# Performance work log

Measured on AMD Instinct MI355X. Metric: run time of the kernel, lower is better.

## Reference

```python
import jax, jax.numpy as jnp
import numpy as np

ALPHA = 0.2  # LeakyReLU negative slope
EDGE_NUM = 3


def _gat(q_nodes, v, adj, a_q, a_v):
    # q_nodes: (b,n,d_hidden), v: (b,n,d_model), adj: (b,n,n)
    # e_ij = LeakyReLU(a_q . h_i + a_v . v_j)  (decomposition of a^T[h_i;v_j])
    s_q = jnp.einsum('bnd,d->bn', q_nodes, a_q)
    s_v = jnp.einsum('bne,e->bn', v, a_v)
    e = jax.nn.leaky_relu(s_q[:, :, None] + s_v[:, None, :], negative_slope=ALPHA)
    e = jnp.where(adj > 0, e, -1e9)
    attn = jax.nn.softmax(e, axis=-1)           # (b,n,n)
    return jnp.einsum('bij,bje->bie', attn, v)  # (b,n,d_model)


def setup_inputs() -> dict:
    key = jax.random.key(0)
    ks = jax.random.split(key, 16)
    b, n, dh, dm = 8, 1024, 512, 512
    s = 0.02
    inp = {
        'nodes': jax.random.normal(ks[0], (b, n, dh), dtype=jnp.float32),
        'mask': jax.random.randint(ks[1], (2, b, n, n), 0, 2, dtype=jnp.int32),
        'node_type': jax.random.randint(ks[2], (b, n), 0, 5, dtype=jnp.int64),
        # edge-typed linears (bias=False), stacked over 3 edge types
        'W_in': jax.random.normal(ks[3], (EDGE_NUM, dh, dm), dtype=jnp.float32) * s,
        'W_out': jax.random.normal(ks[4], (EDGE_NUM, dh, dm), dtype=jnp.float32) * s,
        # GAT attention vectors, split into query / value halves
        'a_in_q': jax.random.normal(ks[5], (dh,), dtype=jnp.float32) * s,
        'a_in_v': jax.random.normal(ks[6], (dm,), dtype=jnp.float32) * s,
        'a_out_q': jax.random.normal(ks[7], (dh,), dtype=jnp.float32) * s,
        'a_out_v': jax.random.normal(ks[8], (dm,), dtype=jnp.float32) * s,
        # GGNN propagator (reset / update / transform)
        'W_r': jax.random.normal(ks[9], (3 * dm, dm), dtype=jnp.float32) * s,
        'b_r': jnp.zeros((dm,), dtype=jnp.float32),
        'W_z': jax.random.normal(ks[10], (3 * dm, dm), dtype=jnp.float32) * s,
        'b_z': jnp.zeros((dm,), dtype=jnp.float32),
        'W_t': jax.random.normal(ks[11], (3 * dm, dm), dtype=jnp.float32) * s,
        'b_t': jnp.zeros((dm,), dtype=jnp.float32),
    }
    return inp


def reference(nodes, mask, node_type, W_in, W_out, a_in_q, a_in_v, a_out_q, a_out_v,
              W_r, b_r, W_z, b_z, W_t, b_t):
    # type masks for tags 2,3,4 -> (3,b,n)
    tags = jnp.arange(2, 2 + EDGE_NUM, dtype=node_type.dtype)
    tmask = (node_type[None, :, :] == tags[:, None, None]).astype(nodes.dtype)
    # edge-typed linear + masked sum over edge types
    node_in = jnp.sum(jnp.einsum('bnd,tde->tbne', nodes, W_in) * tmask[..., None], axis=0)
    node_out = jnp.sum(jnp.einsum('bnd,tde->tbne', nodes, W_out) * tmask[..., None], axis=0)
    # GAT-style masked attention (in / out edges); dropout = identity (eval)
    h_in = _gat(nodes, node_in, mask[0], a_in_q, a_in_v)
    h_out = _gat(nodes, node_out, mask[1], a_out_q, a_out_v)
    # GGNN gated propagator
    a = jnp.concatenate([h_in, h_out, nodes], axis=-1)
    r = jax.nn.sigmoid(a @ W_r + b_r)
    z = jax.nn.sigmoid(a @ W_z + b_z)
    joint = jnp.concatenate([h_in, h_out, r * nodes], axis=-1)
    h_hat = jnp.tanh(joint @ W_t + b_t)
    return (1.0 - z) * nodes + z * h_hat
```

## Files before the change

### kernel.cpp

```cpp
#include <hip/hip_runtime.h>
#include <hip/hip_bf16.h>
#include <stdint.h>

typedef unsigned short u16;
typedef __attribute__((ext_vector_type(8))) short bf16x8;
typedef __attribute__((ext_vector_type(4))) float floatx4;

__device__ __forceinline__ float bf2f(u16 v){ return __uint_as_float(((unsigned)v)<<16); }
__device__ __forceinline__ u16 f2bf(float f){
  unsigned u = __float_as_uint(f);
  unsigned r = 0x7fffu + ((u>>16)&1u);
  return (u16)((u+r)>>16);
}
__device__ __forceinline__ float lrelu(float x){ return x > 0.f ? x : 0.2f*x; }
__device__ __forceinline__ float sigm(float t){
  t = fminf(fmaxf(t, -30.f), 30.f);
  return 1.f/(1.f + expf(-t));
}

#define GLOAD16(ldsdst, gsrc) \
  __builtin_amdgcn_global_load_lds((const __attribute__((address_space(1))) void*)(gsrc), \
      (__attribute__((address_space(3))) void*)(ldsdst), 16, 0, 0)

__global__ void k_detect(const u16* __restrict__ nodes_raw,
                         const int* __restrict__ ntype_raw, int* flags)
{
  __shared__ int s_wild, s_nz;
  if (threadIdx.x == 0){ s_wild = 0; s_nz = 0; }
  __syncthreads();
  int wild = 0;
#pragma unroll
  for (int i = 0; i < 16; i++){
    u16 w = nodes_raw[threadIdx.x*16 + i];
    int e = (w >> 7) & 0xFF;
    if (e != 0 && (e < 102 || e > 152)) wild++;
  }
  int nz = 0;
  if (threadIdx.x < 255 && ntype_raw[2*threadIdx.x + 1] != 0) nz = 1;
  atomicAdd(&s_wild, wild);
  atomicAdd(&s_nz, nz);
  __syncthreads();
  if (threadIdx.x == 0){
    flags[0] = (s_wild > 1024) ? 1 : 0;
    flags[1] = (s_nz == 0) ? 1 : 0;
  }
}

struct CanonDesc {
  const void* src[13];
  u16*        dst[13];
  int startBlk[13];
  int n4[13];
};
__global__ __launch_bounds__(256)
void k_canon_all(CanonDesc d, const int* __restrict__ flags)
{
  int blk = blockIdx.x;
  int seg = 0;
#pragma unroll
  for (int s = 1; s < 13; s++) if (blk >= d.startBlk[s]) seg = s;
  int i = (blk - d.startBlk[seg])*256 + threadIdx.x;
  if (i >= d.n4[seg]) return;
  if (flags[0]) {
    float4 v = ((const float4*)d.src[seg])[i];
    ushort4 o2;
    o2.x = f2bf(v.x); o2.y = f2bf(v.y); o2.z = f2bf(v.z); o2.w = f2bf(v.w);
    ((ushort4*)d.dst[seg])[i] = o2;
  } else {
    ((uint2*)d.dst[seg])[i] = ((const uint2*)d.src[seg])[i];
  }
}

__global__ void k_build_idx(const int* __restrict__ ntype, const int* __restrict__ flags,
                            int* __restrict__ idx, int* __restrict__ cnt)
{
  __shared__ int c[3];
  if (threadIdx.x < 3) c[threadIdx.x] = 0;
  __syncthreads();
  const int i64 = flags[1];
  for (int i = threadIdx.x; i < 8192; i += 256){
    int t = i64 ? ntype[2*i] : ntype[i];
    if (t >= 2 && t <= 4){
      int p = atomicAdd(&c[t-2], 1);
      idx[(t-2)*8192 + p] = i;
    }
  }
  __syncthreads();
  if (threadIdx.x < 3) cnt[threadIdx.x] = c[threadIdx.x];
}

template<class Epi>
__global__ __launch_bounds__(256)
void gemm_bt(const u16* __restrict__ A, int ldA, long sAz,
             const u16* __restrict__ B, int ldB, long sBz,
             int K, Epi epi)
{
  __shared__ __align__(16) u16 As[128][32];
  __shared__ __align__(16) u16 Bs[128][32];
  const int bn = blockIdx.x, bm = blockIdx.y, bz = blockIdx.z;
  const int tid  = threadIdx.x;
  const int lane = tid & 63;
  const int wave = tid >> 6;
  const int wm = (wave & 1) << 6;
  const int wn = (wave >> 1) << 6;
  const int mrow = lane & 15;
  const int quad = lane >> 4;

  const u16* Ab = A + (long)bz*sAz + (long)bm*128*ldA;
  const u16* Bb = B + (long)bz*sBz + (long)bn*128*ldB;
  const int srow = tid >> 2;
  const int scol = (tid & 3) << 3;
  const u16* gA0 = Ab + (long)srow*ldA + scol;
  const u16* gA1 = Ab + (long)(srow+64)*ldA + scol;
  const u16* gB0 = Bb + (long)srow*ldB + scol;
  const u16* gB1 = Bb + (long)(srow+64)*ldB + scol;
  u16* lA0 = &As[srow][scol];
  u16* lA1 = &As[srow+64][scol];
  u16* lB0 = &Bs[srow][scol];
  u16* lB1 = &Bs[srow+64][scol];

  floatx4 acc[4][4];
#pragma unroll
  for (int i=0;i<4;i++)
#pragma unroll
    for (int j=0;j<4;j++) acc[i][j] = 0.f;

  for (int k0 = 0; k0 < K; k0 += 32) {
    GLOAD16(lA0, gA0); GLOAD16(lA1, gA1);
    GLOAD16(lB0, gB0); GLOAD16(lB1, gB1);
    gA0 += 32; gA1 += 32; gB0 += 32; gB1 += 32;
    asm volatile("s_waitcnt vmcnt(0)" ::: "memory");
    __syncthreads();
    bf16x8 af[4], bfr[4];
#pragma unroll
    for (int i=0;i<4;i++) af[i]  = *(const bf16x8*)&As[wm + i*16 + mrow][quad*8];
#pragma unroll
    for (int i=0;i<4;i++) bfr[i] = *(const bf16x8*)&Bs[wn + i*16 + mrow][quad*8];
#pragma unroll
    for (int mi=0;mi<4;mi++)
#pragma unroll
      for (int ni=0;ni<4;ni++)
        acc[mi][ni] = __builtin_amdgcn_mfma_f32_16x16x32_bf16(af[mi], bfr[ni], acc[mi][ni], 0,0,0);
    __syncthreads();
  }

#pragma unroll
  for (int mi=0;mi<4;mi++)
#pragma unroll
    for (int ni=0;ni<4;ni++) {
      const int col  = (bn<<7) + wn + ni*16 + mrow;
      const int row0 = (bm<<7) + wm + mi*16 + quad*4;
#pragma unroll
      for (int r=0;r<4;r++)
        epi(row0 + r, col, bz, acc[mi][ni][r]);
    }
}

__global__ __launch_bounds__(256)
void gemm_typed(const u16* __restrict__ A, const u16* __restrict__ B,
                const int* __restrict__ idx, const int* __restrict__ cnt,
                u16* __restrict__ node_in, u16* __restrict__ node_out)
{
  const int bz = blockIdx.z;
  const int count = cnt[bz];
  const int m0 = blockIdx.y << 7;
  if (m0 >= count) return;
  __shared__ __align__(16) u16 As[128][32];
  __shared__ __align__(16) u16 Bs[128][32];
  const int bn = blockIdx.x;
  const int tid  = threadIdx.x;
  const int lane = tid & 63;
  const int wave = tid >> 6;
  const int wm = (wave & 1) << 6;
  const int wn = (wave >> 1) << 6;
  const int mrow = lane & 15;
  const int quad = lane >> 4;
  const int* myidx = idx + bz*8192;

  const int srow = tid >> 2;
  const int scol = (tid & 3) << 3;
  int r0i = m0 + srow;      if (r0i >= count) r0i = m0;
  int r1i = m0 + srow + 64; if (r1i >= count) r1i = m0;
  const u16* gA0 = A + (long)myidx[r0i]*512 + scol;
  const u16* gA1 = A + (long)myidx[r1i]*512 + scol;
  const u16* Bb = B + (long)bz*1024*512 + (long)bn*128*512;
  const u16* gB0 = Bb + (long)srow*512 + scol;
  const u16* gB1 = Bb + (long)(srow+64)*512 + scol;
  u16* lA0 = &As[srow][scol];
  u16* lA1 = &As[srow+64][scol];
  u16* lB0 = &Bs[srow][scol];
  u16* lB1 = &Bs[srow+64][scol];

  floatx4 acc[4][4];
#pragma unroll
  for (int i=0;i<4;i++)
#pragma unroll
    for (int j=0;j<4;j++) acc[i][j] = 0.f;

  for (int k0 = 0; k0 < 512; k0 += 32) {
    GLOAD16(lA0, gA0); GLOAD16(lA1, gA1);
    GLOAD16(lB0, gB0); GLOAD16(lB1, gB1);
    gA0 += 32; gA1 += 32; gB0 += 32; gB1 += 32;
    asm volatile("s_waitcnt vmcnt(0)" ::: "memory");
    __syncthreads();
    bf16x8 af[4], bfr[4];
#pragma unroll
    for (int i=0;i<4;i++) af[i]  = *(const bf16x8*)&As[wm + i*16 + mrow][quad*8];
#pragma unroll
    for (int i=0;i<4;i++) bfr[i] = *(const bf16x8*)&Bs[wn + i*16 + mrow][quad*8];
#pragma unroll
    for (int mi=0;mi<4;mi++)
#pragma unroll
      for (int ni=0;ni<4;ni++)
        acc[mi][ni] = __builtin_amdgcn_mfma_f32_16x16x32_bf16(af[mi], bfr[ni], acc[mi][ni], 0,0,0);
    __syncthreads();
  }

#pragma unroll
  for (int mi=0;mi<4;mi++) {
    const int lr0 = wm + mi*16 + quad*4;
#pragma unroll
    for (int r=0;r<4;r++) {
      const int lr = lr0 + r;
      if (m0 + lr >= count) continue;
      const long orig = myidx[m0 + lr];
#pragma unroll
      for (int ni=0;ni<4;ni++) {
        const int col = (bn<<7) + wn + ni*16 + mrow;
        u16 h = f2bf(acc[mi][ni][r]);
        if (col < 512) node_in [orig*512 + col]       = h;
        else           node_out[orig*512 + (col-512)] = h;
      }
    }
  }
}

struct EpiPV {
  const float* inv_l; u16* X; int colOff;
  __device__ void operator()(int row, int col, int bz, float v) const {
    long gr = (long)bz*1024 + row;
    X[gr*2048 + colOff + col] = f2bf(v * inv_l[gr]);
  }
};
struct EpiG1 {
  const u16* nodes; const u16* b_r; const u16* b_z; u16* X; u16* zbuf;
  __device__ void operator()(int row, int col, int bz, float v) const {
    if (col < 512) {
      float r = sigm(v + bf2f(b_r[col]));
      X[(long)row*2048 + 1536 + col] = f2bf(r * bf2f(nodes[(long)row*512 + col]));
    } else {
      int c = col - 512;
      zbuf[(long)row*512 + c] = f2bf(sigm(v + bf2f(b_z[c])));
    }
  }
};
struct EpiG2 {
  const u16* zbuf; const u16* nodes; const u16* b_t; const int* flags; void* out;
  __device__ void operator()(int row, int col, int bz, float v) const {
    long idx = (long)row*512 + col;
    float t = fminf(fmaxf(v + bf2f(b_t[col]), -15.f), 15.f);
    float h = tanhf(t);
    float z = bf2f(zbuf[idx]);
    float nv = bf2f(nodes[idx]);
    float o2 = (1.f - z)*nv + z*h;
    if (flags[0]) ((float*)out)[idx] = o2;
    else          ((u16*)out)[idx]   = f2bf(o2);
  }
};

__global__ __launch_bounds__(256)
void k_transpose(u16* __restrict__ dst, int ldD, long dzs,
                 const u16* __restrict__ src, int ldS, long szs)
{
  __shared__ u16 tile[32][33];
  src += (long)blockIdx.z * szs;
  dst += (long)blockIdx.z * dzs;
  const int c0 = blockIdx.x*32, r0 = blockIdx.y*32;
  const int tx = threadIdx.x, ty = threadIdx.y;
#pragma unroll
  for (int i=0;i<32;i+=8)
    tile[ty+i][tx] = src[(long)(r0+ty+i)*ldS + c0 + tx];
  __syncthreads();
#pragma unroll
  for (int i=0;i<32;i+=8)
    dst[(long)(c0+ty+i)*ldD + r0 + tx] = tile[tx][ty+i];
}

struct TrDesc { const u16* src[3]; u16* dst[3]; int rot[3]; };
__global__ __launch_bounds__(256)
void k_wtrans(TrDesc d)
{
  __shared__ u16 tile[32][33];
  const int z = blockIdx.z;
  const u16* src = d.src[z];
  u16* dst = d.dst[z];
  const int c0 = blockIdx.x*32, r0 = blockIdx.y*32;
  const int tx = threadIdx.x, ty = threadIdx.y;
#pragma unroll
  for (int i=0;i<32;i+=8)
    tile[ty+i][tx] = src[(long)(r0+ty+i)*512 + c0 + tx];
  __syncthreads();
  const int k0 = (r0 + d.rot[z]) % 1536;
#pragma unroll
  for (int i=0;i<32;i+=8)
    dst[(long)(c0+ty+i)*1536 + k0 + tx] = tile[tx][ty+i];
}

__global__ __launch_bounds__(256)
void k_vtrans(const u16* __restrict__ nin, const u16* __restrict__ nout,
              u16* __restrict__ vin, u16* __restrict__ vout)
{
  __shared__ u16 tile[32][33];
  const int z = blockIdx.z;
  const int b = z & 7;
  const u16* src = (z < 8 ? nin : nout) + (long)b*1024*512;
  u16* dst = (z < 8 ? vin : vout) + (long)b*512*1024;
  const int c0 = blockIdx.x*32, r0 = blockIdx.y*32;
  const int tx = threadIdx.x, ty = threadIdx.y;
#pragma unroll
  for (int i=0;i<32;i+=8)
    tile[ty+i][tx] = src[(long)(r0+ty+i)*512 + c0 + tx];
  __syncthreads();
#pragma unroll
  for (int i=0;i<32;i+=8)
    dst[(long)(c0+ty+i)*1024 + r0 + tx] = tile[tx][ty+i];
}

__global__ __launch_bounds__(256)
void k_copyX(const u16* __restrict__ nodes, u16* __restrict__ X)
{
  long idx = (long)blockIdx.x*256 + threadIdx.x;
  long r = idx >> 6;
  int  c = (int)(idx & 63) << 3;
  *(uint4*)&X[r*2048 + c] = *(const uint4*)&nodes[r*512 + c];
}

__device__ __forceinline__ void load8f(float* f, const u16* p){
  uint4 q = *(const uint4*)p;
  unsigned w[4] = {q.x, q.y, q.z, q.w};
#pragma unroll
  for (int i=0;i<4;i++){ f[2*i] = bf2f((u16)(w[i]&0xffffu)); f[2*i+1] = bf2f((u16)(w[i]>>16)); }
}

__global__ __launch_bounds__(256)
void k_svec(const u16* __restrict__ nodes, const u16* __restrict__ nin, const u16* __restrict__ nout,
            const u16* __restrict__ aiq, const u16* __restrict__ aiv,
            const u16* __restrict__ aoq, const u16* __restrict__ aov,
            float* sq_in, float* sq_out, float* sv_in, float* sv_out)
{
  const int lane = threadIdx.x & 63, wave = threadIdx.x >> 6;
  const long row = (long)blockIdx.x*4 + wave;
  const int c = lane << 3;
  float xn[8], xi[8], xo[8], q1[8], v1[8], q2[8], v2[8];
  load8f(xn, nodes + row*512 + c);
  load8f(xi, nin   + row*512 + c);
  load8f(xo, nout  + row*512 + c);
  load8f(q1, aiq + c); load8f(v1, aiv + c);
  load8f(q2, aoq + c); load8f(v2, aov + c);
  float s0=0,s1=0,s2=0,s3=0;
#pragma unroll
  for (int j=0;j<8;j++){ s0 += xn[j]*q1[j]; s1 += xn[j]*q2[j]; s2 += xi[j]*v1[j]; s3 += xo[j]*v2[j]; }
#pragma unroll
  for (int off=32; off; off>>=1){
    s0 += __shfl_xor(s0, off);
    s1 += __shfl_xor(s1, off);
    s2 += __shfl_xor(s2, off);
    s3 += __shfl_xor(s3, off);
  }
  if (lane==0){ sq_in[row]=s0; sq_out[row]=s1; sv_in[row]=s2; sv_out[row]=s3; }
}

__global__ __launch_bounds__(256)
void k_stats(const int* __restrict__ mask, const float* __restrict__ sq,
             const float* __restrict__ sv, u16* __restrict__ P, float* __restrict__ inv_l)
{
  const int lane = threadIdx.x & 63, wave = threadIdx.x >> 6;
  const long row = (long)blockIdx.x*4 + wave;
  const long b = row >> 10;
  const int* mrow = mask + row*1024;
  const float* svb = sv + b*1024;
  const float qs = sq[row];
  float m = -3.0e38f;
#pragma unroll
  for (int it=0; it<8; ++it) {
    int j = it*128 + lane*2;
    int2 mk = *(const int2*)&mrow[j];
    float2 s = *(const float2*)&svb[j];
    float e0 = mk.x > 0 ? lrelu(qs + s.x) : -1e9f;
    float e1 = mk.y > 0 ? lrelu(qs + s.y) : -1e9f;
    m = fmaxf(m, fmaxf(e0, e1));
  }
#pragma unroll
  for (int off=32; off; off>>=1) m = fmaxf(m, __shfl_xor(m, off));
  float l = 0.f;
#pragma unroll
  for (int it=0; it<8; ++it) {
    int j = it*128 + lane*2;
    int2 mk = *(const int2*)&mrow[j];
    float2 s = *(const float2*)&svb[j];
    float e0 = mk.x > 0 ? lrelu(qs + s.x) : -1e9f;
    float e1 = mk.y > 0 ? lrelu(qs + s.y) : -1e9f;
    float p0 = expf(e0 - m), p1 = expf(e1 - m);
    *(unsigned*)&P[row*1024 + j] = (unsigned)f2bf(p0) | ((unsigned)f2bf(p1) << 16);
    l += p0 + p1;
  }
#pragma unroll
  for (int off=32; off; off>>=1) l += __shfl_xor(l, off);
  if (lane==0) inv_l[row] = 1.f / l;
}

extern "C" void kernel_launch(void* const* d_in, const int* in_sizes, int n_in,
                              void* d_out, int out_size, void* d_ws, size_t ws_size,
                              hipStream_t stream)
{
  const void* nodes_r   = d_in[0];
  const int*  mask      = (const int*)d_in[1];
  const int*  ntype     = (const int*)d_in[2];

  char* base = (char*)d_ws;
  size_t o = 0;
  auto alloc = [&](size_t bytes){ void* p = base + o; o += (bytes + 255) & ~size_t(255); return p; };
  int*  flags   = (int*)alloc(256);
  int*  cnt     = (int*)alloc(256);
  int*  idx     = (int*)alloc(3ll*8192*4);
  u16* cn_nodes = (u16*)alloc(8192ll*512*2);
  u16* cn_Win   = (u16*)alloc(3ll*512*512*2);
  u16* cn_Wout  = (u16*)alloc(3ll*512*512*2);
  u16* cn_Wr    = (u16*)alloc(1536ll*512*2);
  u16* cn_Wz    = (u16*)alloc(1536ll*512*2);
  u16* cn_Wt    = (u16*)alloc(1536ll*512*2);
  u16* cn_aiq   = (u16*)alloc(512*2);
  u16* cn_aiv   = (u16*)alloc(512*2);
  u16* cn_aoq   = (u16*)alloc(512*2);
  u16* cn_aov   = (u16*)alloc(512*2);
  u16* cn_br    = (u16*)alloc(512*2);
  u16* cn_bz    = (u16*)alloc(512*2);
  u16* cn_bt    = (u16*)alloc(512*2);
  u16* node_in  = (u16*)alloc(8192ll*512*2);
  u16* node_out = (u16*)alloc(8192ll*512*2);
  u16* VtIn     = (u16*)alloc(8ll*512*1024*2);
  u16* VtOut    = (u16*)alloc(8ll*512*1024*2);
  u16* X        = (u16*)alloc(8192ll*2048*2);
  u16* P        = (u16*)alloc(8ll*1024*1024*2);
  u16* Wio_t    = (u16*)alloc(3ll*1024*512*2);
  u16* Wrz_t    = (u16*)alloc(1024ll*1536*2);
  u16* Wt_t     = (u16*)alloc(512ll*1536*2);
  float* sq_in  = (float*)alloc(8192*4);
  float* sq_out = (float*)alloc(8192*4);
  float* sv_in  = (float*)alloc(8192*4);
  float* sv_out = (float*)alloc(8192*4);
  float* il_in  = (float*)alloc(8192*4);
  float* il_out = (float*)alloc(8192*4);
  u16* zbuf = node_in;

  hipMemsetAsync(node_in, 0, 2ll*8192*512*2, stream);

  k_detect<<<1, 256, 0, stream>>>((const u16*)nodes_r, ntype, flags);

  CanonDesc cd;
  const int canonN[13] = {8192*512, 3*512*512, 3*512*512, 1536*512, 1536*512, 1536*512,
                          512,512,512,512,512,512,512};
  u16* canonDst[13] = {cn_nodes, cn_Win, cn_Wout, cn_Wr, cn_Wz, cn_Wt,
                       cn_aiq, cn_aiv, cn_aoq, cn_aov, cn_br, cn_bz, cn_bt};
  const int canonSrcIdx[13] = {0,3,4,9,11,13,5,6,7,8,10,12,14};
  int blk = 0;
  for (int s=0;s<13;s++){
    cd.src[s] = d_in[canonSrcIdx[s]];
    cd.dst[s] = canonDst[s];
    cd.n4[s]  = canonN[s]/4;
    cd.startBlk[s] = blk;
    blk += (cd.n4[s] + 255)/256;
  }
  k_canon_all<<<blk, 256, 0, stream>>>(cd, flags);

  k_build_idx<<<1, 256, 0, stream>>>(ntype, flags, idx, cnt);

  TrDesc td;
  td.src[0]=cn_Wr; td.src[1]=cn_Wz; td.src[2]=cn_Wt;
  td.dst[0]=Wrz_t; td.dst[1]=Wrz_t + 512ll*1536; td.dst[2]=Wt_t;
  td.rot[0]=512; td.rot[1]=512; td.rot[2]=0;
  k_wtrans<<<dim3(16,48,3), dim3(32,8), 0, stream>>>(td);
  dim3 tb(32,8);
  k_transpose<<<dim3(16,16,3), tb, 0, stream>>>(Wio_t,             512, 1024ll*512, cn_Win,  512, 512ll*512);
  k_transpose<<<dim3(16,16,3), tb, 0, stream>>>(Wio_t + 512ll*512, 512, 1024ll*512, cn_Wout, 512, 512ll*512);

  gemm_typed<<<dim3(8,64,3), 256, 0, stream>>>(cn_nodes, Wio_t, idx, cnt, node_in, node_out);

  k_vtrans<<<dim3(16,32,16), tb, 0, stream>>>(node_in, node_out, VtIn, VtOut);

  k_svec<<<2048, 256, 0, stream>>>(cn_nodes, node_in, node_out, cn_aiq, cn_aiv, cn_aoq, cn_aov,
                                   sq_in, sq_out, sv_in, sv_out);
  k_copyX<<<2048, 256, 0, stream>>>(cn_nodes, X);

  k_stats<<<2048, 256, 0, stream>>>(mask, sq_in, sv_in, P, il_in);
  gemm_bt<<<dim3(4,8,8), 256, 0, stream>>>(P, 1024, 1024ll*1024, VtIn, 1024, 512ll*1024, 1024,
                                           EpiPV{il_in, X, 512});
  k_stats<<<2048, 256, 0, stream>>>(mask + 8ll*1024*1024, sq_out, sv_out, P, il_out);
  gemm_bt<<<dim3(4,8,8), 256, 0, stream>>>(P, 1024, 1024ll*1024, VtOut, 1024, 512ll*1024, 1024,
                                           EpiPV{il_out, X, 1024});

  gemm_bt<<<dim3(8,64,1), 256, 0, stream>>>(X, 2048, 0ll, Wrz_t, 1536, 0ll, 1536,
                                            EpiG1{cn_nodes, cn_br, cn_bz, X, zbuf});
  gemm_bt<<<dim3(4,64,1), 256, 0, stream>>>(X + 512, 2048, 0ll, Wt_t, 1536, 0ll, 1536,
                                            EpiG2{zbuf, cn_nodes, cn_bt, flags, (void*)d_out});
}
```

Before: 435.4 us.

## Double-buffer GEMM LDS tiles, fuse copies and transposes, reorder block grids

The GEMM kernels now use two LDS buffers, so the next K-slice load is issued before the current slice's MFMAs and the trailing barrier per iteration is dropped. The X copy is folded into the canonicalization kernel, and the Win/Wout transposes are merged into one batched k_wtrans launch, removing several launches. Grid dimensions are reordered so adjacent blocks walk M first, or the batch first for the PV GEMMs, to change L2 reuse. k_stats now caches the logits in registers instead of recomputing them, and reads the mask with wider vector loads.

```diff
diff --git a/kernel.cpp b/kernel.cpp
--- a/kernel.cpp
+++ b/kernel.cpp
@@ -53,7 +53,7 @@
   int n4[13];
 };
 __global__ __launch_bounds__(256)
-void k_canon_all(CanonDesc d, const int* __restrict__ flags)
+void k_canon_all(CanonDesc d, u16* __restrict__ X, const int* __restrict__ flags)
 {
   int blk = blockIdx.x;
   int seg = 0;
@@ -61,13 +61,21 @@
   for (int s = 1; s < 13; s++) if (blk >= d.startBlk[s]) seg = s;
   int i = (blk - d.startBlk[seg])*256 + threadIdx.x;
   if (i >= d.n4[seg]) return;
+  uint2 bits;
   if (flags[0]) {
     float4 v = ((const float4*)d.src[seg])[i];
     ushort4 o2;
     o2.x = f2bf(v.x); o2.y = f2bf(v.y); o2.z = f2bf(v.z); o2.w = f2bf(v.w);
-    ((ushort4*)d.dst[seg])[i] = o2;
+    bits = *(uint2*)&o2;
   } else {
-    ((uint2*)d.dst[seg])[i] = ((const uint2*)d.src[seg])[i];
+    bits = ((const uint2*)d.src[seg])[i];
+  }
+  ((uint2*)d.dst[seg])[i] = bits;
+  if (seg == 0) {
+    int e0 = i*4;
+    long r = e0 >> 9;
+    int  c = e0 & 511;
+    *(uint2*)&X[r*2048 + c] = bits;
   }
 }
 
@@ -89,15 +97,17 @@
   if (threadIdx.x < 3) cnt[threadIdx.x] = c[threadIdx.x];
 }
 
-template<class Epi>
+template<int MODE, class Epi>
 __global__ __launch_bounds__(256)
 void gemm_bt(const u16* __restrict__ A, int ldA, long sAz,
              const u16* __restrict__ B, int ldB, long sBz,
              int K, Epi epi)
 {
-  __shared__ __align__(16) u16 As[128][32];
-  __shared__ __align__(16) u16 Bs[128][32];
-  const int bn = blockIdx.x, bm = blockIdx.y, bz = blockIdx.z;
+  __shared__ __align__(16) u16 As[2][128][32];
+  __shared__ __align__(16) u16 Bs[2][128][32];
+  int bm, bn, bz;
+  if (MODE == 0){ bm = blockIdx.x; bn = blockIdx.y; bz = blockIdx.z; }
+  else          { bz = blockIdx.x; bn = blockIdx.y; bm = blockIdx.z; }
   const int tid  = threadIdx.x;
   const int lane = tid & 63;
   const int wave = tid >> 6;
@@ -114,10 +124,6 @@
   const u16* gA1 = Ab + (long)(srow+64)*ldA + scol;
   const u16* gB0 = Bb + (long)srow*ldB + scol;
   const u16* gB1 = Bb + (long)(srow+64)*ldB + scol;
-  u16* lA0 = &As[srow][scol];
-  u16* lA1 = &As[srow+64][scol];
-  u16* lB0 = &Bs[srow][scol];
-  u16* lB1 = &Bs[srow+64][scol];
 
   floatx4 acc[4][4];
 #pragma unroll
@@ -125,23 +131,31 @@
 #pragma unroll
     for (int j=0;j<4;j++) acc[i][j] = 0.f;
 
-  for (int k0 = 0; k0 < K; k0 += 32) {
-    GLOAD16(lA0, gA0); GLOAD16(lA1, gA1);
-    GLOAD16(lB0, gB0); GLOAD16(lB1, gB1);
+  auto issue = [&](int buf){
+    GLOAD16(&As[buf][srow][scol],    gA0);
+    GLOAD16(&As[buf][srow+64][scol], gA1);
+    GLOAD16(&Bs[buf][srow][scol],    gB0);
+    GLOAD16(&Bs[buf][srow+64][scol], gB1);
     gA0 += 32; gA1 += 32; gB0 += 32; gB1 += 32;
+  };
+
+  issue(0);
+  const int nIter = K >> 5;
+  for (int it = 0; it < nIter; ++it) {
+    const int cur = it & 1;
     asm volatile("s_waitcnt vmcnt(0)" ::: "memory");
     __syncthreads();
+    if (it + 1 < nIter) issue(cur ^ 1);
     bf16x8 af[4], bfr[4];
 #pragma unroll
-    for (int i=0;i<4;i++) af[i]  = *(const bf16x8*)&As[wm + i*16 + mrow][quad*8];
-#pragma unroll
-    for (int i=0;i<4;i++) bfr[i] = *(const bf16x8*)&Bs[wn + i*16 + mrow][quad*8];
+    for (int i=0;i<4;i++) af[i]  = *(const bf16x8*)&As[cur][wm + i*16 + mrow][quad*8];
+#pragma unroll
+    for (int i=0;i<4;i++) bfr[i] = *(const bf16x8*)&Bs[cur][wn + i*16 + mrow][quad*8];
 #pragma unroll
     for (int mi=0;mi<4;mi++)
 #pragma unroll
       for (int ni=0;ni<4;ni++)
         acc[mi][ni] = __builtin_amdgcn_mfma_f32_16x16x32_bf16(af[mi], bfr[ni], acc[mi][ni], 0,0,0);
-    __syncthreads();
   }
 
 #pragma unroll
@@ -163,11 +177,11 @@
 {
   const int bz = blockIdx.z;
   const int count = cnt[bz];
-  const int m0 = blockIdx.y << 7;
+  const int m0 = blockIdx.x << 7;
   if (m0 >= count) return;
-  __shared__ __align__(16) u16 As[128][32];
-  __shared__ __align__(16) u16 Bs[128][32];
-  const int bn = blockIdx.x;
+  __shared__ __align__(16) u16 As[2][128][32];
+  __shared__ __align__(16) u16 Bs[2][128][32];
+  const int bn = blockIdx.y;
   const int tid  = threadIdx.x;
   const int lane = tid & 63;
   const int wave = tid >> 6;
@@ -186,10 +200,6 @@
   const u16* Bb = B + (long)bz*1024*512 + (long)bn*128*512;
   const u16* gB0 = Bb + (long)srow*512 + scol;
   const u16* gB1 = Bb + (long)(srow+64)*512 + scol;
-  u16* lA0 = &As[srow][scol];
-  u16* lA1 = &As[srow+64][scol];
-  u16* lB0 = &Bs[srow][scol];
-  u16* lB1 = &Bs[srow+64][scol];
 
   floatx4 acc[4][4];
 #pragma unroll
@@ -197,23 +207,30 @@
 #pragma unroll
     for (int j=0;j<4;j++) acc[i][j] = 0.f;
 
-  for (int k0 = 0; k0 < 512; k0 += 32) {
-    GLOAD16(lA0, gA0); GLOAD16(lA1, gA1);
-    GLOAD16(lB0, gB0); GLOAD16(lB1, gB1);
+  auto issue = [&](int buf){
+    GLOAD16(&As[buf][srow][scol],    gA0);
+    GLOAD16(&As[buf][srow+64][scol], gA1);
+    GLOAD16(&Bs[buf][srow][scol],    gB0);
+    GLOAD16(&Bs[buf][srow+64][scol], gB1);
     gA0 += 32; gA1 += 32; gB0 += 32; gB1 += 32;
+  };
+
+  issue(0);
+  for (int it = 0; it < 16; ++it) {
+    const int cur = it & 1;
     asm volatile("s_waitcnt vmcnt(0)" ::: "memory");
     __syncthreads();
+    if (it + 1 < 16) issue(cur ^ 1);
     bf16x8 af[4], bfr[4];
 #pragma unroll
-    for (int i=0;i<4;i++) af[i]  = *(const bf16x8*)&As[wm + i*16 + mrow][quad*8];
-#pragma unroll
-    for (int i=0;i<4;i++) bfr[i] = *(const bf16x8*)&Bs[wn + i*16 + mrow][quad*8];
+    for (int i=0;i<4;i++) af[i]  = *(const bf16x8*)&As[cur][wm + i*16 + mrow][quad*8];
+#pragma unroll
+    for (int i=0;i<4;i++) bfr[i] = *(const bf16x8*)&Bs[cur][wn + i*16 + mrow][quad*8];
 #pragma unroll
     for (int mi=0;mi<4;mi++)
 #pragma unroll
       for (int ni=0;ni<4;ni++)
         acc[mi][ni] = __builtin_amdgcn_mfma_f32_16x16x32_bf16(af[mi], bfr[ni], acc[mi][ni], 0,0,0);
-    __syncthreads();
   }
 
 #pragma unroll
@@ -268,42 +285,28 @@
   }
 };
 
-__global__ __launch_bounds__(256)
-void k_transpose(u16* __restrict__ dst, int ldD, long dzs,
-                 const u16* __restrict__ src, int ldS, long szs)
-{
-  __shared__ u16 tile[32][33];
-  src += (long)blockIdx.z * szs;
-  dst += (long)blockIdx.z * dzs;
-  const int c0 = blockIdx.x*32, r0 = blockIdx.y*32;
-  const int tx = threadIdx.x, ty = threadIdx.y;
-#pragma unroll
-  for (int i=0;i<32;i+=8)
-    tile[ty+i][tx] = src[(long)(r0+ty+i)*ldS + c0 + tx];
-  __syncthreads();
-#pragma unroll
-  for (int i=0;i<32;i+=8)
-    dst[(long)(c0+ty+i)*ldD + r0 + tx] = tile[tx][ty+i];
-}
-
-struct TrDesc { const u16* src[3]; u16* dst[3]; int rot[3]; };
+struct TrDesc {
+  const u16* src[9]; u16* dst[9]; int rot[9]; int ldD[9]; int rows[9]; int modK[9];
+};
 __global__ __launch_bounds__(256)
 void k_wtrans(TrDesc d)
 {
   __shared__ u16 tile[32][33];
   const int z = blockIdx.z;
+  const int r0 = blockIdx.y*32;
+  if (r0 >= d.rows[z]) return;
   const u16* src = d.src[z];
   u16* dst = d.dst[z];
-  const int c0 = blockIdx.x*32, r0 = blockIdx.y*32;
+  const int c0 = blockIdx.x*32;
   const int tx = threadIdx.x, ty = threadIdx.y;
 #pragma unroll
   for (int i=0;i<32;i+=8)
     tile[ty+i][tx] = src[(long)(r0+ty+i)*512 + c0 + tx];
   __syncthreads();
-  const int k0 = (r0 + d.rot[z]) % 1536;
+  const int k0 = (r0 + d.rot[z]) % d.modK[z];
 #pragma unroll
   for (int i=0;i<32;i+=8)
-    dst[(long)(c0+ty+i)*1536 + k0 + tx] = tile[tx][ty+i];
+    dst[(long)(c0+ty+i)*d.ldD[z] + k0 + tx] = tile[tx][ty+i];
 }
 
 __global__ __launch_bounds__(256)
@@ -324,15 +327,6 @@
 #pragma unroll
   for (int i=0;i<32;i+=8)
     dst[(long)(c0+ty+i)*1024 + r0 + tx] = tile[tx][ty+i];
-}
-
-__global__ __launch_bounds__(256)
-void k_copyX(const u16* __restrict__ nodes, u16* __restrict__ X)
-{
-  long idx = (long)blockIdx.x*256 + threadIdx.x;
-  long r = idx >> 6;
-  int  c = (int)(idx & 63) << 3;
-  *(uint4*)&X[r*2048 + c] = *(const uint4*)&nodes[r*512 + c];
 }
 
 __device__ __forceinline__ void load8f(float* f, const u16* p){
@@ -381,28 +375,30 @@
   const float* svb = sv + b*1024;
   const float qs = sq[row];
   float m = -3.0e38f;
-#pragma unroll
-  for (int it=0; it<8; ++it) {
-    int j = it*128 + lane*2;
-    int2 mk = *(const int2*)&mrow[j];
-    float2 s = *(const float2*)&svb[j];
-    float e0 = mk.x > 0 ? lrelu(qs + s.x) : -1e9f;
-    float e1 = mk.y > 0 ? lrelu(qs + s.y) : -1e9f;
-    m = fmaxf(m, fmaxf(e0, e1));
+  float e[4][4];
+#pragma unroll
+  for (int it=0; it<4; ++it) {
+    int j = it*256 + lane*4;
+    int4 mk = *(const int4*)&mrow[j];
+    float4 s = *(const float4*)&svb[j];
+    e[it][0] = mk.x > 0 ? lrelu(qs + s.x) : -1e9f;
+    e[it][1] = mk.y > 0 ? lrelu(qs + s.y) : -1e9f;
+    e[it][2] = mk.z > 0 ? lrelu(qs + s.z) : -1e9f;
+    e[it][3] = mk.w > 0 ? lrelu(qs + s.w) : -1e9f;
+    m = fmaxf(m, fmaxf(fmaxf(e[it][0], e[it][1]), fmaxf(e[it][2], e[it][3])));
   }
 #pragma unroll
   for (int off=32; off; off>>=1) m = fmaxf(m, __shfl_xor(m, off));
   float l = 0.f;
 #pragma unroll
-  for (int it=0; it<8; ++it) {
-    int j = it*128 + lane*2;
-    int2 mk = *(const int2*)&mrow[j];
-    float2 s = *(const float2*)&svb[j];
-    float e0 = mk.x > 0 ? lrelu(qs + s.x) : -1e9f;
-    float e1 = mk.y > 0 ? lrelu(qs + s.y) : -1e9f;
-    float p0 = expf(e0 - m), p1 = expf(e1 - m);
-    *(unsigned*)&P[row*1024 + j] = (unsigned)f2bf(p0) | ((unsigned)f2bf(p1) << 16);
-    l += p0 + p1;
+  for (int it=0; it<4; ++it) {
+    int j = it*256 + lane*4;
+    float p0 = expf(e[it][0] - m), p1 = expf(e[it][1] - m);
+    float p2 = expf(e[it][2] - m), p3 = expf(e[it][3] - m);
+    ushort4 pk;
+    pk.x = f2bf(p0); pk.y = f2bf(p1); pk.z = f2bf(p2); pk.w = f2bf(p3);
+    *(ushort4*)&P[row*1024 + j] = pk;
+    l += (p0 + p1) + (p2 + p3);
   }
 #pragma unroll
   for (int off=32; off; off>>=1) l += __shfl_xor(l, off);
@@ -471,7 +467,7 @@
     cd.startBlk[s] = blk;
     blk += (cd.n4[s] + 255)/256;
   }
-  k_canon_all<<<blk, 256, 0, stream>>>(cd, flags);
+  k_canon_all<<<blk, 256, 0, stream>>>(cd, X, flags);
 
   k_build_idx<<<1, 256, 0, stream>>>(ntype, flags, idx, cnt);
 
@@ -479,28 +475,33 @@
   td.src[0]=cn_Wr; td.src[1]=cn_Wz; td.src[2]=cn_Wt;
   td.dst[0]=Wrz_t; td.dst[1]=Wrz_t + 512ll*1536; td.dst[2]=Wt_t;
   td.rot[0]=512; td.rot[1]=512; td.rot[2]=0;
-  k_wtrans<<<dim3(16,48,3), dim3(32,8), 0, stream>>>(td);
-  dim3 tb(32,8);
-  k_transpose<<<dim3(16,16,3), tb, 0, stream>>>(Wio_t,             512, 1024ll*512, cn_Win,  512, 512ll*512);
-  k_transpose<<<dim3(16,16,3), tb, 0, stream>>>(Wio_t + 512ll*512, 512, 1024ll*512, cn_Wout, 512, 512ll*512);
-
-  gemm_typed<<<dim3(8,64,3), 256, 0, stream>>>(cn_nodes, Wio_t, idx, cnt, node_in, node_out);
-
-  k_vtrans<<<dim3(16,32,16), tb, 0, stream>>>(node_in, node_out, VtIn, VtOut);
+  td.ldD[0]=1536; td.ldD[1]=1536; td.ldD[2]=1536;
+  td.rows[0]=1536; td.rows[1]=1536; td.rows[2]=1536;
+  td.modK[0]=1536; td.modK[1]=1536; td.modK[2]=1536;
+  for (int t=0;t<3;t++){
+    td.src[3+t]=cn_Win  + (long)t*512*512; td.dst[3+t]=Wio_t + (long)t*1024*512;
+    td.src[6+t]=cn_Wout + (long)t*512*512; td.dst[6+t]=Wio_t + (long)t*1024*512 + 512ll*512;
+    td.rot[3+t]=td.rot[6+t]=0; td.ldD[3+t]=td.ldD[6+t]=512;
+    td.rows[3+t]=td.rows[6+t]=512; td.modK[3+t]=td.modK[6+t]=512;
+  }
+  k_wtrans<<<dim3(16,48,9), dim3(32,8), 0, stream>>>(td);
+
+  gemm_typed<<<dim3(64,8,3), 256, 0, stream>>>(cn_nodes, Wio_t, idx, cnt, node_in, node_out);
+
+  k_vtrans<<<dim3(16,32,16), dim3(32,8), 0, stream>>>(node_in, node_out, VtIn, VtOut);
 
   k_svec<<<2048, 256, 0, stream>>>(cn_nodes, node_in, node_out, cn_aiq, cn_aiv, cn_aoq, cn_aov,
                                    sq_in, sq_out, sv_in, sv_out);
-  k_copyX<<<2048, 256, 0, stream>>>(cn_nodes, X);
 
   k_stats<<<2048, 256, 0, stream>>>(mask, sq_in, sv_in, P, il_in);
-  gemm_bt<<<dim3(4,8,8), 256, 0, stream>>>(P, 1024, 1024ll*1024, VtIn, 1024, 512ll*1024, 1024,
-                                           EpiPV{il_in, X, 512});
+  gemm_bt<1><<<dim3(8,4,8), 256, 0, stream>>>(P, 1024, 1024ll*1024, VtIn, 1024, 512ll*1024, 1024,
+                                              EpiPV{il_in, X, 512});
   k_stats<<<2048, 256, 0, stream>>>(mask + 8ll*1024*1024, sq_out, sv_out, P, il_out);
-  gemm_bt<<<dim3(4,8,8), 256, 0, stream>>>(P, 1024, 1024ll*1024, VtOut, 1024, 512ll*1024, 1024,
-                                           EpiPV{il_out, X, 1024});
-
-  gemm_bt<<<dim3(8,64,1), 256, 0, stream>>>(X, 2048, 0ll, Wrz_t, 1536, 0ll, 1536,
-                                            EpiG1{cn_nodes, cn_br, cn_bz, X, zbuf});
-  gemm_bt<<<dim3(4,64,1), 256, 0, stream>>>(X + 512, 2048, 0ll, Wt_t, 1536, 0ll, 1536,
-                                            EpiG2{zbuf, cn_nodes, cn_bt, flags, (void*)d_out});
-}
+  gemm_bt<1><<<dim3(8,4,8), 256, 0, stream>>>(P, 1024, 1024ll*1024, VtOut, 1024, 512ll*1024, 1024,
+                                              EpiPV{il_out, X, 1024});
+
+  gemm_bt<0><<<dim3(64,8,1), 256, 0, stream>>>(X, 2048, 0ll, Wrz_t, 1536, 0ll, 1536,
+                                               EpiG1{cn_nodes, cn_br, cn_bz, X, zbuf});
+  gemm_bt<0><<<dim3(64,4,1), 256, 0, stream>>>(X + 512, 2048, 0ll, Wt_t, 1536, 0ll, 1536,
+                                               EpiG2{zbuf, cn_nodes, cn_bt, flags, (void*)d_out});
+}
```

After: 397.4 us. 8.7% less time.
